# Kernel optimization log

Hardware: AMD Instinct MI355X
Metric: run time of the kernel (lower is better)

## Reference

```python
import jax, jax.numpy as jnp
import numpy as np

B, P, K = 8, 1024, 20          # clouds, points per cloud, knn neighbors
H, HD = 256, 512               # module hidden_dim, edge-MLP hidden (TransformerBlockRes default)
L, C = 3, 512                  # n_hidden_layers, n_components
N = B * P
LN_EPS = 1e-5


def _layer_norm(x, g, b):
    m = jnp.mean(x, axis=-1, keepdims=True)
    v = jnp.var(x, axis=-1, keepdims=True)
    return (x - m) * jax.lax.rsqrt(v + LN_EPS) * g + b


def _mlp(x, W1, b1, g1, be1, W2, b2, g2, be2):
    # Linear -> LayerNorm -> ELU -> Linear -> LayerNorm -> ELU (pos_nn / attn_nn)
    h = jax.nn.elu(_layer_norm(x @ W1 + b1, g1, be1))
    return jax.nn.elu(_layer_norm(h @ W2 + b2, g2, be2))


def _knn(pos):
    # knn_graph within each cloud, loop=False (self excluded). Equal-size clouds.
    p = pos.reshape(B, P, 3)
    d2 = jnp.sum((p[:, :, None, :] - p[:, None, :, :]) ** 2, axis=-1)  # [B,P,P]
    d2 = d2 + jnp.eye(P, dtype=d2.dtype) * 1e10                        # exclude self
    idx = jax.lax.top_k(-d2, K)[1]                                     # [B,P,K]
    return (idx + (jnp.arange(B) * P)[:, None, None]).reshape(N, K)    # global ids


def setup_inputs() -> dict:
    key = jax.random.key(0)
    cnt = [0]

    def nrm(shape, scale):
        cnt[0] += 1
        return (jax.random.normal(jax.random.fold_in(key, cnt[0]), shape, dtype=jnp.float32) * scale)

    d = {}
    d["pos"] = nrm((N, 3), 1.0)
    d["batch"] = jnp.repeat(jnp.arange(B, dtype=jnp.int32), P)
    # stem Linear(3, H)
    d["ffm_W"] = nrm((3, H), 3 ** -0.5); d["ffm_b"] = jnp.zeros((H,), jnp.float32)
    # PointTransformerConv linears (no bias), stacked over L layers
    s = H ** -0.5
    d["lin_W"] = nrm((L, H, H), s); d["src_W"] = nrm((L, H, H), s); d["dst_W"] = nrm((L, H, H), s)
    # pos_nn: Linear(3,HD)+LN+ELU+Linear(HD,H)+LN+ELU
    d["pos1_W"] = nrm((L, 3, HD), 3 ** -0.5); d["pos1_b"] = jnp.zeros((L, HD), jnp.float32)
    d["pos_ln1_g"] = jnp.ones((L, HD), jnp.float32); d["pos_ln1_b"] = jnp.zeros((L, HD), jnp.float32)
    d["pos2_W"] = nrm((L, HD, H), HD ** -0.5); d["pos2_b"] = jnp.zeros((L, H), jnp.float32)
    d["pos_ln2_g"] = jnp.ones((L, H), jnp.float32); d["pos_ln2_b"] = jnp.zeros((L, H), jnp.float32)
    # attn_nn: Linear(H,HD)+LN+ELU+Linear(HD,H)+LN+ELU
    d["att1_W"] = nrm((L, H, HD), s); d["att1_b"] = jnp.zeros((L, HD), jnp.float32)
    d["att_ln1_g"] = jnp.ones((L, HD), jnp.float32); d["att_ln1_b"] = jnp.zeros((L, HD), jnp.float32)
    d["att2_W"] = nrm((L, HD, H), HD ** -0.5); d["att2_b"] = jnp.zeros((L, H), jnp.float32)
    d["att_ln2_g"] = jnp.ones((L, H), jnp.float32); d["att_ln2_b"] = jnp.zeros((L, H), jnp.float32)
    # per-layer tail: LayerNorm + ELU + Linear + ResidualCoefficient
    d["blk_ln_g"] = jnp.ones((L, H), jnp.float32); d["blk_ln_b"] = jnp.zeros((L, H), jnp.float32)
    d["blk_W"] = nrm((L, H, H), s); d["blk_b"] = jnp.zeros((L, H), jnp.float32)
    d["res_alpha"] = nrm((L,), 0.1)  # torch init is zeros; small random for a nontrivial test
    d["r1_W"] = nrm((H, H), s); d["r1_b"] = jnp.zeros((H,), jnp.float32)
    d["r2_W"] = nrm((H, H), s); d["r2_b"] = jnp.zeros((H,), jnp.float32)
    d["r2_ln_g"] = jnp.ones((H,), jnp.float32); d["r2_ln_b"] = jnp.zeros((H,), jnp.float32)
    d["r3_W"] = nrm((H, H), s); d["r3_b"] = jnp.zeros((H,), jnp.float32)
    d["r3_ln_g"] = jnp.ones((H,), jnp.float32); d["r3_ln_b"] = jnp.zeros((H,), jnp.float32)
    d["r4_W"] = nrm((H, C), s); d["r4_b"] = jnp.zeros((C,), jnp.float32)
    return d


def reference(pos, batch, ffm_W, ffm_b, lin_W, src_W, dst_W,
              pos1_W, pos1_b, pos_ln1_g, pos_ln1_b, pos2_W, pos2_b, pos_ln2_g, pos_ln2_b,
              att1_W, att1_b, att_ln1_g, att_ln1_b, att2_W, att2_b, att_ln2_g, att_ln2_b,
              blk_ln_g, blk_ln_b, blk_W, blk_b, res_alpha,
              r1_W, r1_b, r2_W, r2_b, r2_ln_g, r2_ln_b, r3_W, r3_b, r3_ln_g, r3_ln_b, r4_W, r4_b):
    # knn graph is identical every layer (pos never changes) -> compute once
    neigh = _knn(pos)                       # [N,K] neighbor (source) ids j for each target i
    rel = pos[:, None, :] - pos[neigh]      # pos_i - pos_j, [N,K,3]
    x = pos @ ffm_W + ffm_b                 # [N,H]
    for i in range(L):
        a_src = x @ src_W[i]                # [N,H]
        a_dst = x @ dst_W[i]
        v = x @ lin_W[i]
        delta = _mlp(rel, pos1_W[i], pos1_b[i], pos_ln1_g[i], pos_ln1_b[i],
                     pos2_W[i], pos2_b[i], pos_ln2_g[i], pos_ln2_b[i])          # [N,K,H]
        alpha = _mlp(a_dst[:, None, :] - a_src[neigh] + delta,
                     att1_W[i], att1_b[i], att_ln1_g[i], att_ln1_b[i],
                     att2_W[i], att2_b[i], att_ln2_g[i], att_ln2_b[i])          # [N,K,H]
        attn = jax.nn.softmax(alpha, axis=1)                                    # per-channel over K neighbors
        agg = jnp.sum(attn * (v[neigh] + delta), axis=1)                        # sum aggregation (PyG default)
        h = jax.nn.elu(_layer_norm(agg, blk_ln_g[i], blk_ln_b[i])) @ blk_W[i] + blk_b[i]
        x = x + res_alpha[i] * h
    h = x @ r1_W + r1_b                                                         # [N,H]
    pooled = jax.ops.segment_max(h, batch, num_segments=B)                      # global_max_pool [B,H]
    h = jax.nn.elu(_layer_norm(pooled @ r2_W + r2_b, r2_ln_g, r2_ln_b))
    h = jax.nn.elu(_layer_norm(h @ r3_W + r3_b, r3_ln_g, r3_ln_b))
    return h @ r4_W + r4_b                                                      # [B,C]
```

## Files before the change

kernel.cpp:

```cpp
#include <hip/hip_runtime.h>
#include <math.h>

#define NPTS 8192
#define PPC  1024
#define BCL  8
#define KNN  20
#define HDIM 256
#define HD2  512
#define NL   3
#define NCOMP 512
#define EDG  (NPTS*KNN)
#define QS   768

typedef __bf16 bf16x8 __attribute__((ext_vector_type(8)));
typedef float f32x4 __attribute__((ext_vector_type(4)));
typedef unsigned int uint4v __attribute__((ext_vector_type(4)));
typedef unsigned short us8 __attribute__((ext_vector_type(8)));

__device__ inline unsigned short f2bf(float f) {
  unsigned u = __float_as_uint(f);
  u += 0x7FFF + ((u >> 16) & 1);
  return (unsigned short)(u >> 16);
}
__device__ inline unsigned short f2bf_fast(float f) {
  return (unsigned short)((__float_as_uint(f) + 0x8000u) >> 16);
}
__device__ inline unsigned pack2bf(float a, float b) {
#if __has_builtin(__builtin_amdgcn_cvt_pk_bf16_f32)
  auto t = __builtin_amdgcn_cvt_pk_bf16_f32(a, b);
  return __builtin_bit_cast(unsigned, t);
#else
  return ((__float_as_uint(a) + 0x8000u) >> 16) |
         ((__float_as_uint(b) + 0x8000u) & 0xFFFF0000u);
#endif
}
__device__ inline float bf2f(unsigned short u) {
  return __uint_as_float((unsigned)u << 16);
}
__device__ inline float elu(float y) { return (y > 0.f) ? y : (__expf(y) - 1.f); }

__global__ __launch_bounds__(256)
void knn_wave(const float* __restrict__ pos, int* __restrict__ neigh,
              float* __restrict__ rel_f) {
  __shared__ float px[PPC], py[PPC], pz[PPC];
  int tid = threadIdx.x;
  int i0 = blockIdx.x * 4;
  int base = i0 & ~(PPC - 1);
  for (int t = tid; t < PPC; t += 256) {
    px[t] = pos[(size_t)(base + t) * 3 + 0];
    py[t] = pos[(size_t)(base + t) * 3 + 1];
    pz[t] = pos[(size_t)(base + t) * 3 + 2];
  }
  __syncthreads();
  int wave = tid >> 6, lane = tid & 63;
  int i = i0 + wave;
  int il = i - base;
  float xi = px[il], yi = py[il], zi = pz[il];
  float d[16];
  #pragma unroll
  for (int q = 0; q < 16; ++q) {
    int t = lane + 64 * q;
    float dx = xi - px[t], dy = yi - py[t], dz = zi - pz[t];
    float dd = dx * dx + dy * dy + dz * dz;
    d[q] = (t == il) ? 3.4e38f : dd;
  }
  int mywin = 0;
  for (int k = 0; k < KNN; ++k) {
    float v = d[0]; int idx = lane;
    #pragma unroll
    for (int q = 1; q < 16; ++q)
      if (d[q] < v) { v = d[q]; idx = q * 64 + lane; }
    #pragma unroll
    for (int off = 1; off < 64; off <<= 1) {
      float ov = __shfl_xor(v, off, 64);
      int oi = __shfl_xor(idx, off, 64);
      if (ov < v || (ov == v && oi < idx)) { v = ov; idx = oi; }
    }
    if (lane == k) mywin = idx;
    int qwin = idx >> 6;
    bool own = (idx & 63) == lane;
    #pragma unroll
    for (int q = 0; q < 16; ++q)
      if (own && q == qwin) d[q] = 3.4e38f;
  }
  if (lane < KNN) {
    neigh[(size_t)i * KNN + lane] = base + mywin;
    size_t rb = ((size_t)i * KNN + lane) * 3;
    rel_f[rb + 0] = xi - px[mywin];
    rel_f[rb + 1] = yi - py[mywin];
    rel_f[rb + 2] = zi - pz[mywin];
  }
}

__global__ __launch_bounds__(256)
void transpose_w(const float* __restrict__ W, unsigned short* __restrict__ out,
                 int K, int N, int Kpad) {
  int n = blockIdx.x;
  for (int k = threadIdx.x; k < Kpad; k += 256)
    out[(size_t)n * Kpad + k] = (k < K) ? f2bf(W[(size_t)k * N + n]) : (unsigned short)0;
}

__global__ __launch_bounds__(64)
void pack_w(const float* __restrict__ W, unsigned short* __restrict__ out, int N) {
  int blk = blockIdx.x;
  int NT = N / 16;
  int ks = blk / NT, nt = blk % NT;
  int lane = threadIdx.x;
  int l16 = lane & 15, quad = lane >> 4;
  int col = nt * 16 + l16;
  int krow = ks * 32 + quad * 8;
  unsigned short o[8];
  #pragma unroll
  for (int j = 0; j < 8; ++j)
    o[j] = f2bf(W[(size_t)(krow + j) * N + col]);
  *(uint4v*)&out[((size_t)blk * 64 + lane) * 8] = *(uint4v*)o;
}

__global__ __launch_bounds__(256)
void prep_pos(const float* __restrict__ pos, unsigned short* __restrict__ posb) {
  int idx = blockIdx.x * 256 + threadIdx.x;
  int m = idx >> 5, c = idx & 31;
  posb[idx] = (c < 3) ? f2bf(pos[(size_t)m * 3 + c]) : (unsigned short)0;
}

__global__ __launch_bounds__(256)
void pos_fused(const float* __restrict__ rel_f, const float* __restrict__ W1,
               const float* __restrict__ b1, const float* __restrict__ g1,
               const float* __restrict__ be1,
               const unsigned short* __restrict__ B2p, const float* __restrict__ bias2,
               const float* __restrict__ g2, const float* __restrict__ be2,
               unsigned short* __restrict__ delta_b, int edge_base) {
  __shared__ alignas(16) char smem[46464];
  unsigned short* H = (unsigned short*)smem;
  float* w1s = (float*)(smem + 33280);
  float* b1s = w1s + 1536;
  float* g1s = b1s + 512;
  float* be1s = g1s + 512;
  float* lnsum = (float*)(smem + 45568);
  float* lnsq = lnsum + 64;
  float* relS = (float*)(smem + 46080);
  int tid = threadIdx.x;
  int wave = tid >> 6, lane = tid & 63;
  int el0 = blockIdx.x * 32;
  int eg0 = edge_base + el0;
  for (int t = tid; t < 1536; t += 256) w1s[t] = W1[t];
  for (int t = tid; t < 512; t += 256) { b1s[t] = b1[t]; g1s[t] = g1[t]; be1s[t] = be1[t]; }
  if (tid < 96) relS[tid] = rel_f[(size_t)eg0 * 3 + tid];
  __syncthreads();
  {
    int rIW = lane >> 3, sub = lane & 7;
    int row = wave * 8 + rIW;
    float r0 = relS[row * 3 + 0], r1v = relS[row * 3 + 1], r2v = relS[row * 3 + 2];
    int cb = sub * 64;
    float h[64]; float s = 0.f, sq = 0.f;
    #pragma unroll
    for (int cc = 0; cc < 16; ++cc) {
      f32x4 w0 = *(const f32x4*)&w1s[cb + cc * 4];
      f32x4 wa = *(const f32x4*)&w1s[512 + cb + cc * 4];
      f32x4 wb = *(const f32x4*)&w1s[1024 + cb + cc * 4];
      f32x4 bb = *(const f32x4*)&b1s[cb + cc * 4];
      #pragma unroll
      for (int q = 0; q < 4; ++q) {
        float hv = fmaf(r0, w0[q], fmaf(r1v, wa[q], fmaf(r2v, wb[q], bb[q])));
        h[cc * 4 + q] = hv; s += hv; sq += hv * hv;
      }
    }
    #pragma unroll
    for (int off = 1; off < 8; off <<= 1) { s += __shfl_xor(s, off, 64); sq += __shfl_xor(sq, off, 64); }
    float mean = s * (1.f / 512.f);
    float var = sq * (1.f / 512.f) - mean * mean;
    float rr = rsqrtf(var + 1e-5f);
    #pragma unroll
    for (int cc = 0; cc < 8; ++cc) {
      unsigned u[4];
      #pragma unroll
      for (int q = 0; q < 4; ++q) {
        int c0 = cb + cc * 8 + 2 * q;
        float y0 = elu((h[cc * 8 + 2 * q]     - mean) * rr * g1s[c0]     + be1s[c0]);
        float y1 = elu((h[cc * 8 + 2 * q + 1] - mean) * rr * g1s[c0 + 1] + be1s[c0 + 1]);
        u[q] = pack2bf(y0, y1);
      }
      *(uint4v*)&H[row * 520 + cb + cc * 8] = *(uint4v*)u;
    }
  }
  __syncthreads();
  int quad = lane >> 4, l16 = lane & 15;
  int wm2 = (wave >> 1) * 16, wn2 = (wave & 1) * 128, wni = wave & 1;
  int nb2 = (wave & 1) * 8;
  f32x4 acc2[8] = {};
  for (int k0 = 0; k0 < 512; k0 += 32) {
    int ks = k0 >> 5;
    bf16x8 bvv[8];
    #pragma unroll
    for (int ni = 0; ni < 8; ++ni)
      bvv[ni] = *(const bf16x8*)(B2p + ((size_t)(ks * 16 + nb2 + ni) * 64 + lane) * 8);
    bf16x8 a2 = __builtin_bit_cast(bf16x8, *(const uint4v*)&H[(wm2 + l16) * 520 + k0 + quad * 8]);
    #pragma unroll
    for (int ni = 0; ni < 8; ++ni)
      acc2[ni] = __builtin_amdgcn_mfma_f32_16x16x32_bf16(a2, bvv[ni], acc2[ni], 0, 0, 0);
  }
  #pragma unroll
  for (int r = 0; r < 4; ++r) {
    int row = wm2 + quad * 4 + r;
    float s2 = 0.f, q2 = 0.f;
    #pragma unroll
    for (int ni = 0; ni < 8; ++ni) {
      float val = acc2[ni][r] + bias2[wn2 + ni * 16 + l16];
      acc2[ni][r] = val; s2 += val; q2 += val * val;
    }
    #pragma unroll
    for (int off = 1; off < 16; off <<= 1) { s2 += __shfl_xor(s2, off, 64); q2 += __shfl_xor(q2, off, 64); }
    if (l16 == 0) { lnsum[wni * 32 + row] = s2; lnsq[wni * 32 + row] = q2; }
  }
  __syncthreads();
  #pragma unroll
  for (int r = 0; r < 4; ++r) {
    int row = wm2 + quad * 4 + r;
    float tot = lnsum[row] + lnsum[32 + row];
    float tsq = lnsq[row] + lnsq[32 + row];
    float mean = tot * (1.f / 256.f);
    float var = tsq * (1.f / 256.f) - mean * mean;
    float rr = rsqrtf(var + 1e-5f);
    size_t ob = (size_t)(el0 + row) * 256;
    #pragma unroll
    for (int ni = 0; ni < 8; ++ni) {
      int col = wn2 + ni * 16 + l16;
      delta_b[ob + col] = f2bf_fast(elu((acc2[ni][r] - mean) * rr * g2[col] + be2[col]));
    }
  }
}

__global__ __launch_bounds__(256)
void attn_fused(const unsigned short* __restrict__ qkv,
                const unsigned short* __restrict__ delta_b,
                const int* __restrict__ neigh,
                const unsigned short* __restrict__ B1p, const float* __restrict__ bias1,
                const float* __restrict__ g1, const float* __restrict__ be1,
                const unsigned short* __restrict__ B2p, const float* __restrict__ bias2,
                const float* __restrict__ g2, const float* __restrict__ be2,
                unsigned short* __restrict__ alpha_b, int edge_base) {
  __shared__ alignas(16) char smem[34304];
  unsigned short* H = (unsigned short*)smem;
  float* lnsum = (float*)(smem + 33280);
  float* lnsq  = lnsum + 64;
  int* iS = (int*)(smem + 33792);
  int* jS = iS + 32;
  int tid = threadIdx.x;
  int wave = tid >> 6, lane = tid & 63;
  int quad = lane >> 4, l16 = lane & 15;
  int el0 = blockIdx.x * 32;
  int eg0 = edge_base + el0;
  if (tid < 32) { iS[tid] = (eg0 + tid) / KNN; jS[tid] = neigh[eg0 + tid]; }
  __syncthreads();
  int wm1 = (wave >> 1) * 16, wn1 = (wave & 1) * 256, wni = wave & 1;
  int nb1 = (wave & 1) * 16;
  us8 areg[8];
  {
    int r = wm1 + l16;
    int i = iS[r], j = jS[r], e = el0 + r;
    const unsigned short* pdp = qkv + (size_t)i * QS + 256;
    const unsigned short* psp = qkv + (size_t)j * QS;
    const unsigned short* plp = delta_b + (size_t)e * 256;
    #pragma unroll
    for (int ks = 0; ks < 8; ++ks) {
      int c = ks * 32 + quad * 8;
      us8 pd = *(const us8*)(pdp + c);
      us8 ps = *(const us8*)(psp + c);
      us8 pl = *(const us8*)(plp + c);
      unsigned u[4];
      #pragma unroll
      for (int q = 0; q < 4; ++q)
        u[q] = pack2bf(bf2f(pd[2*q])   - bf2f(ps[2*q])   + bf2f(pl[2*q]),
                       bf2f(pd[2*q+1]) - bf2f(ps[2*q+1]) + bf2f(pl[2*q+1]));
      areg[ks] = __builtin_bit_cast(us8, *(uint4v*)u);
    }
  }
  f32x4 acc1[16] = {};
  #pragma unroll
  for (int ks = 0; ks < 8; ++ks) {
    bf16x8 bvv[16];
    #pragma unroll
    for (int ni = 0; ni < 16; ++ni)
      bvv[ni] = *(const bf16x8*)(B1p + ((size_t)(ks * 32 + nb1 + ni) * 64 + lane) * 8);
    bf16x8 a1 = __builtin_bit_cast(bf16x8, areg[ks]);
    #pragma unroll
    for (int ni = 0; ni < 16; ++ni)
      acc1[ni] = __builtin_amdgcn_mfma_f32_16x16x32_bf16(a1, bvv[ni], acc1[ni], 0, 0, 0);
  }
  #pragma unroll
  for (int r = 0; r < 4; ++r) {
    int row = wm1 + quad * 4 + r;
    float s = 0.f, sq = 0.f;
    #pragma unroll
    for (int ni = 0; ni < 16; ++ni) {
      float val = acc1[ni][r] + bias1[wn1 + ni * 16 + l16];
      acc1[ni][r] = val; s += val; sq += val * val;
    }
    #pragma unroll
    for (int off = 1; off < 16; off <<= 1) { s += __shfl_xor(s, off, 64); sq += __shfl_xor(sq, off, 64); }
    if (l16 == 0) { lnsum[wni * 32 + row] = s; lnsq[wni * 32 + row] = sq; }
  }
  __syncthreads();
  #pragma unroll
  for (int r = 0; r < 4; ++r) {
    int row = wm1 + quad * 4 + r;
    float tot = lnsum[row] + lnsum[32 + row];
    float tsq = lnsq[row] + lnsq[32 + row];
    float mean = tot * (1.f / 512.f);
    float var = tsq * (1.f / 512.f) - mean * mean;
    float rr = rsqrtf(var + 1e-5f);
    #pragma unroll
    for (int ni = 0; ni < 16; ++ni) {
      int col = wn1 + ni * 16 + l16;
      H[row * 520 + col] = f2bf_fast(elu((acc1[ni][r] - mean) * rr * g1[col] + be1[col]));
    }
  }
  __syncthreads();
  int wm2 = (wave >> 1) * 16, wn2 = (wave & 1) * 128;
  int nb2 = (wave & 1) * 8;
  f32x4 acc2[8] = {};
  for (int k0 = 0; k0 < 512; k0 += 32) {
    int ks = k0 >> 5;
    bf16x8 bvv[8];
    #pragma unroll
    for (int ni = 0; ni < 8; ++ni)
      bvv[ni] = *(const bf16x8*)(B2p + ((size_t)(ks * 16 + nb2 + ni) * 64 + lane) * 8);
    bf16x8 a2 = __builtin_bit_cast(bf16x8, *(const uint4v*)&H[(wm2 + l16) * 520 + k0 + quad * 8]);
    #pragma unroll
    for (int ni = 0; ni < 8; ++ni)
      acc2[ni] = __builtin_amdgcn_mfma_f32_16x16x32_bf16(a2, bvv[ni], acc2[ni], 0, 0, 0);
  }
  #pragma unroll
  for (int r = 0; r < 4; ++r) {
    int row = wm2 + quad * 4 + r;
    float s2 = 0.f, q2 = 0.f;
    #pragma unroll
    for (int ni = 0; ni < 8; ++ni) {
      float val = acc2[ni][r] + bias2[wn2 + ni * 16 + l16];
      acc2[ni][r] = val; s2 += val; q2 += val * val;
    }
    #pragma unroll
    for (int off = 1; off < 16; off <<= 1) { s2 += __shfl_xor(s2, off, 64); q2 += __shfl_xor(q2, off, 64); }
    if (l16 == 0) { lnsum[wni * 32 + row] = s2; lnsq[wni * 32 + row] = q2; }
  }
  __syncthreads();
  #pragma unroll
  for (int r = 0; r < 4; ++r) {
    int row = wm2 + quad * 4 + r;
    float tot = lnsum[row] + lnsum[32 + row];
    float tsq = lnsq[row] + lnsq[32 + row];
    float mean = tot * (1.f / 256.f);
    float var = tsq * (1.f / 256.f) - mean * mean;
    float rr = rsqrtf(var + 1e-5f);
    size_t ob = (size_t)(el0 + row) * 256;
    #pragma unroll
    for (int ni = 0; ni < 8; ++ni) {
      int col = wn2 + ni * 16 + l16;
      alpha_b[ob + col] = f2bf_fast(elu((acc2[ni][r] - mean) * rr * g2[col] + be2[col]));
    }
  }
}

#define APAD 40
__global__ __launch_bounds__(256)
void gemm_mfma(const unsigned short* __restrict__ A, const unsigned short* __restrict__ Bt,
               const float* __restrict__ bias, float* __restrict__ Cf,
               unsigned short* __restrict__ Cb, int M, int Nn, int Kk) {
  __shared__ alignas(16) unsigned short As[128 * APAD];
  __shared__ alignas(16) unsigned short Bs[128 * APAD];
  int tid = threadIdx.x;
  int wave = tid >> 6, lane = tid & 63;
  int quad = lane >> 4, l16 = lane & 15;
  int wm = (wave >> 1) * 64, wn = (wave & 1) * 64;
  int m0 = blockIdx.y * 128, n0 = blockIdx.x * 128;
  f32x4 acc[4][4] = {};
  int srow = tid >> 2;
  int scol = (tid & 3) * 8;
  for (int k0 = 0; k0 < Kk; k0 += 32) {
    #pragma unroll
    for (int h = 0; h < 2; ++h) {
      int r = srow + h * 64;
      int gm = m0 + r;
      uint4v va = {0, 0, 0, 0};
      if (gm < M) va = *(const uint4v*)(A + (size_t)gm * Kk + k0 + scol);
      *(uint4v*)(&As[r * APAD + scol]) = va;
      int gn = n0 + r;
      uint4v vb = *(const uint4v*)(Bt + (size_t)gn * Kk + k0 + scol);
      *(uint4v*)(&Bs[r * APAD + scol]) = vb;
    }
    __syncthreads();
    bf16x8 af[4], bfr[4];
    #pragma unroll
    for (int mi = 0; mi < 4; ++mi)
      af[mi] = __builtin_bit_cast(bf16x8, *(const uint4v*)(&As[(wm + mi * 16 + l16) * APAD + quad * 8]));
    #pragma unroll
    for (int ni = 0; ni < 4; ++ni)
      bfr[ni] = __builtin_bit_cast(bf16x8, *(const uint4v*)(&Bs[(wn + ni * 16 + l16) * APAD + quad * 8]));
    #pragma unroll
    for (int mi = 0; mi < 4; ++mi)
      #pragma unroll
      for (int ni = 0; ni < 4; ++ni)
        acc[mi][ni] = __builtin_amdgcn_mfma_f32_16x16x32_bf16(af[mi], bfr[ni], acc[mi][ni], 0, 0, 0);
    __syncthreads();
  }
  float bvs[4]; int gns[4];
  #pragma unroll
  for (int ni = 0; ni < 4; ++ni) {
    gns[ni] = n0 + wn + ni * 16 + l16;
    bvs[ni] = bias ? bias[gns[ni]] : 0.f;
  }
  #pragma unroll
  for (int mi = 0; mi < 4; ++mi) {
    #pragma unroll
    for (int r = 0; r < 4; ++r) {
      int gm = m0 + wm + mi * 16 + quad * 4 + r;
      if (gm >= M) continue;
      #pragma unroll
      for (int ni = 0; ni < 4; ++ni) {
        float val = acc[mi][ni][r] + bvs[ni];
        if (Cf) Cf[(size_t)gm * Nn + gns[ni]] = val;
        if (Cb) Cb[(size_t)gm * Nn + gns[ni]] = f2bf_fast(val);
      }
    }
  }
}

#define BM0 64
#define BN0 64
#define BK0 16
__global__ __launch_bounds__(256)
void gemm_bias(const float* __restrict__ A, const float* __restrict__ Bw,
               const float* __restrict__ bias, float* __restrict__ C,
               int M, int Nn, int Kk) {
  __shared__ float Asm[BK0][BM0 + 1];
  __shared__ float Bsm[BK0][BN0 + 1];
  int bm = blockIdx.y * BM0, bn = blockIdx.x * BN0;
  int tid = threadIdx.x;
  int tx = tid & 15, ty = tid >> 4;
  float acc[4][4] = {{0.f}};
  for (int k0 = 0; k0 < Kk; k0 += BK0) {
    #pragma unroll
    for (int ii = 0; ii < 4; ++ii) {
      int e = tid + ii * 256;
      int m = e >> 4, k = e & 15;
      int gm = bm + m, gk = k0 + k;
      Asm[k][m] = (gm < M && gk < Kk) ? A[(size_t)gm * Kk + gk] : 0.f;
    }
    #pragma unroll
    for (int ii = 0; ii < 4; ++ii) {
      int e = tid + ii * 256;
      int k = e >> 6, n = e & 63;
      int gk = k0 + k, gn = bn + n;
      Bsm[k][n] = (gk < Kk && gn < Nn) ? Bw[(size_t)gk * Nn + gn] : 0.f;
    }
    __syncthreads();
    #pragma unroll
    for (int kk = 0; kk < BK0; ++kk) {
      float a[4], b[4];
      #pragma unroll
      for (int ii = 0; ii < 4; ++ii) a[ii] = Asm[kk][ty * 4 + ii];
      #pragma unroll
      for (int jj = 0; jj < 4; ++jj) b[jj] = Bsm[kk][tx * 4 + jj];
      #pragma unroll
      for (int ii = 0; ii < 4; ++ii)
        #pragma unroll
        for (int jj = 0; jj < 4; ++jj)
          acc[ii][jj] += a[ii] * b[jj];
    }
    __syncthreads();
  }
  #pragma unroll
  for (int ii = 0; ii < 4; ++ii) {
    int gm = bm + ty * 4 + ii;
    if (gm >= M) continue;
    #pragma unroll
    for (int jj = 0; jj < 4; ++jj) {
      int gn = bn + tx * 4 + jj;
      if (gn >= Nn) continue;
      float vv = acc[ii][jj];
      if (bias) vv += bias[gn];
      C[(size_t)gm * Nn + gn] = vv;
    }
  }
}

__global__ __launch_bounds__(256)
void ln_elu_kernel(const float* __restrict__ in, float* __restrict__ outf,
                   unsigned short* __restrict__ outb,
                   const float* __restrict__ g, const float* __restrict__ bb,
                   int Cn, int do_elu) {
  __shared__ float sdata[4];
  size_t row = blockIdx.x;
  const float* x = in + row * Cn;
  int tid = threadIdx.x;
  float v0 = x[tid];
  float v1 = (Cn == 512) ? x[tid + 256] : 0.f;
  float s = v0 + v1;
  #pragma unroll
  for (int off = 32; off > 0; off >>= 1) s += __shfl_xor(s, off, 64);
  if ((tid & 63) == 0) sdata[tid >> 6] = s;
  __syncthreads();
  float mean = (sdata[0] + sdata[1] + sdata[2] + sdata[3]) / (float)Cn;
  float d0 = v0 - mean;
  float d1 = (Cn == 512) ? (v1 - mean) : 0.f;
  float sq = d0 * d0 + d1 * d1;
  __syncthreads();
  #pragma unroll
  for (int off = 32; off > 0; off >>= 1) sq += __shfl_xor(sq, off, 64);
  if ((tid & 63) == 0) sdata[tid >> 6] = sq;
  __syncthreads();
  float var = (sdata[0] + sdata[1] + sdata[2] + sdata[3]) / (float)Cn;
  float r = rsqrtf(var + 1e-5f);
  float y0 = d0 * r * g[tid] + bb[tid];
  if (do_elu) y0 = elu(y0);
  if (outf) outf[row * Cn + tid] = y0;
  if (outb) outb[row * Cn + tid] = f2bf_fast(y0);
  if (Cn == 512) {
    float y1 = d1 * r * g[tid + 256] + bb[tid + 256];
    if (do_elu) y1 = elu(y1);
    if (outf) outf[row * Cn + tid + 256] = y1;
    if (outb) outb[row * Cn + tid + 256] = f2bf_fast(y1);
  }
}

__global__ __launch_bounds__(256)
void softmax_agg(const unsigned short* __restrict__ alpha_b,
                 const unsigned short* __restrict__ delta_b,
                 const unsigned short* __restrict__ qkv,
                 const int* __restrict__ neigh,
                 float* __restrict__ agg, int node0) {
  int nl = blockIdx.x;
  int c = threadIdx.x;
  int i = node0 + nl;
  float av[KNN];
  float mx = -3.4e38f;
  #pragma unroll
  for (int k = 0; k < KNN; ++k) {
    av[k] = bf2f(alpha_b[((size_t)nl * KNN + k) * HDIM + c]);
    mx = fmaxf(mx, av[k]);
  }
  float ssum = 0.f;
  #pragma unroll
  for (int k = 0; k < KNN; ++k) { av[k] = __expf(av[k] - mx); ssum += av[k]; }
  float inv = 1.f / ssum;
  float acc = 0.f;
  #pragma unroll
  for (int k = 0; k < KNN; ++k) {
    int j = neigh[(size_t)i * KNN + k];
    acc += av[k] * inv * (bf2f(qkv[(size_t)j * QS + 512 + c]) +
                          bf2f(delta_b[((size_t)nl * KNN + k) * HDIM + c]));
  }
  agg[(size_t)i * HDIM + c] = acc;
}

__global__ __launch_bounds__(256)
void axpy_res(float* __restrict__ x, unsigned short* __restrict__ xb,
              const float* __restrict__ h, const float* __restrict__ alpha, int l) {
  size_t idx = (size_t)blockIdx.x * 256 + threadIdx.x;
  float nv = x[idx] + alpha[l] * h[idx];
  x[idx] = nv;
  xb[idx] = f2bf_fast(nv);
}

__global__ __launch_bounds__(256)
void seg_max_p(const float* __restrict__ h, float* __restrict__ part) {
  int blk = blockIdx.x;
  int b = blk >> 4, ch = blk & 15;
  int c = threadIdx.x;
  const float* base = h + ((size_t)b * PPC + (size_t)ch * 64) * HDIM;
  float m = -3.4e38f;
  for (int p = 0; p < 64; ++p)
    m = fmaxf(m, base[(size_t)p * HDIM + c]);
  part[(size_t)blk * HDIM + c] = m;
}
__global__ __launch_bounds__(256)
void seg_max_f(const float* __restrict__ part, float* __restrict__ pooled) {
  int b = blockIdx.x;
  int c = threadIdx.x;
  float m = -3.4e38f;
  for (int k = 0; k < 16; ++k)
    m = fmaxf(m, part[(size_t)(b * 16 + k) * HDIM + c]);
  pooled[(size_t)b * HDIM + c] = m;
}

extern "C" void kernel_launch(void* const* d_in, const int* in_sizes, int n_in,
                              void* d_out, int out_size, void* d_ws, size_t ws_size,
                              hipStream_t stream) {
  const float* pos       = (const float*)d_in[0];
  const float* ffm_W     = (const float*)d_in[2];
  const float* ffm_b     = (const float*)d_in[3];
  const float* lin_W     = (const float*)d_in[4];
  const float* src_W     = (const float*)d_in[5];
  const float* dst_W     = (const float*)d_in[6];
  const float* pos1_W    = (const float*)d_in[7];
  const float* pos1_b    = (const float*)d_in[8];
  const float* pos_ln1_g = (const float*)d_in[9];
  const float* pos_ln1_b = (const float*)d_in[10];
  const float* pos2_W    = (const float*)d_in[11];
  const float* pos2_b    = (const float*)d_in[12];
  const float* pos_ln2_g = (const float*)d_in[13];
  const float* pos_ln2_b = (const float*)d_in[14];
  const float* att1_W    = (const float*)d_in[15];
  const float* att1_b    = (const float*)d_in[16];
  const float* att_ln1_g = (const float*)d_in[17];
  const float* att_ln1_b = (const float*)d_in[18];
  const float* att2_W    = (const float*)d_in[19];
  const float* att2_b    = (const float*)d_in[20];
  const float* att_ln2_g = (const float*)d_in[21];
  const float* att_ln2_b = (const float*)d_in[22];
  const float* blk_ln_g  = (const float*)d_in[23];
  const float* blk_ln_b  = (const float*)d_in[24];
  const float* blk_W     = (const float*)d_in[25];
  const float* blk_b     = (const float*)d_in[26];
  const float* res_alpha = (const float*)d_in[27];
  const float* r1_W = (const float*)d_in[28]; const float* r1_b = (const float*)d_in[29];
  const float* r2_W = (const float*)d_in[30]; const float* r2_b = (const float*)d_in[31];
  const float* r2_ln_g = (const float*)d_in[32]; const float* r2_ln_b = (const float*)d_in[33];
  const float* r3_W = (const float*)d_in[34]; const float* r3_b = (const float*)d_in[35];
  const float* r3_ln_g = (const float*)d_in[36]; const float* r3_ln_b = (const float*)d_in[37];
  const float* r4_W = (const float*)d_in[38]; const float* r4_b = (const float*)d_in[39];
  float* out = (float*)d_out;

  char* wsp = (char*)d_ws;
  auto alloc = [&](size_t bytes) -> void* {
    void* p = (void*)wsp;
    wsp += (bytes + 255) & ~(size_t)255;
    return p;
  };
  int*            neigh   = (int*)alloc(EDG * sizeof(int));
  float*          rel_f   = (float*)alloc((size_t)EDG * 3 * 4);
  unsigned short* posb    = (unsigned short*)alloc((size_t)NPTS * 32 * 2);
  float*          x       = (float*)alloc((size_t)NPTS * HDIM * 4);
  unsigned short* xb      = (unsigned short*)alloc((size_t)NPTS * HDIM * 2);
  unsigned short* xln_b   = (unsigned short*)alloc((size_t)NPTS * HDIM * 2);
  unsigned short* qkv     = (unsigned short*)alloc((size_t)NPTS * QS * 2);
  float*          agg     = (float*)alloc((size_t)NPTS * HDIM * 4);
  float*          segp    = (float*)alloc((size_t)128 * HDIM * 4);
  float*          pooled  = (float*)alloc((size_t)BCL * HDIM * 4);
  float*          hh      = (float*)alloc((size_t)BCL * HDIM * 4);
  unsigned short* ffmt = (unsigned short*)alloc((size_t)HDIM * 32 * 2);
  unsigned short* r1t  = (unsigned short*)alloc((size_t)HDIM * HDIM * 2);
  unsigned short *qkvt[NL], *blkt[NL];
  unsigned short *pos2p[NL], *att1p[NL], *att2p[NL];
  for (int l = 0; l < NL; ++l) {
    qkvt[l]  = (unsigned short*)alloc((size_t)QS * HDIM * 2);
    blkt[l]  = (unsigned short*)alloc((size_t)HDIM * HDIM * 2);
    pos2p[l] = (unsigned short*)alloc((size_t)HDIM * HD2 * 2);
    att1p[l] = (unsigned short*)alloc((size_t)HD2 * HDIM * 2);
    att2p[l] = (unsigned short*)alloc((size_t)HDIM * HD2 * 2);
  }
  size_t used = (size_t)(wsp - (char*)d_ws);
  size_t avail = (ws_size > used) ? (ws_size - used) : 0;
  size_t per_node = (size_t)KNN * (HDIM * 2 * 2) + 1024;
  int Nc = (int)(avail / per_node);
  if (Nc > NPTS) Nc = NPTS;
  Nc &= ~15;
  if (Nc < 16) Nc = 16;
  unsigned short* delta_b = (unsigned short*)alloc((size_t)Nc * KNN * HDIM * 2);
  unsigned short* alpha_b = (unsigned short*)alloc((size_t)Nc * KNN * HDIM * 2);

  auto mgemm = [&](const unsigned short* A, const unsigned short* Bt, const float* bias,
                   float* Cf, unsigned short* Cb, int M, int Nn, int Kk) {
    dim3 g(Nn / 128, (M + 127) / 128);
    gemm_mfma<<<g, dim3(256), 0, stream>>>(A, Bt, bias, Cf, Cb, M, Nn, Kk);
  };
  auto fgemm = [&](const float* A, const float* Bw, const float* bias, float* Cp,
                   int M, int Nn, int Kk) {
    dim3 g((Nn + BN0 - 1) / BN0, (M + BM0 - 1) / BM0);
    gemm_bias<<<g, dim3(256), 0, stream>>>(A, Bw, bias, Cp, M, Nn, Kk);
  };

  transpose_w<<<HDIM, 256, 0, stream>>>(ffm_W, ffmt, 3, HDIM, 32);
  transpose_w<<<HDIM, 256, 0, stream>>>(r1_W, r1t, HDIM, HDIM, HDIM);
  for (int l = 0; l < NL; ++l) {
    transpose_w<<<HDIM, 256, 0, stream>>>(src_W + (size_t)l * HDIM * HDIM, qkvt[l], HDIM, HDIM, HDIM);
    transpose_w<<<HDIM, 256, 0, stream>>>(dst_W + (size_t)l * HDIM * HDIM, qkvt[l] + 256 * 256, HDIM, HDIM, HDIM);
    transpose_w<<<HDIM, 256, 0, stream>>>(lin_W + (size_t)l * HDIM * HDIM, qkvt[l] + 512 * 256, HDIM, HDIM, HDIM);
    transpose_w<<<HDIM, 256, 0, stream>>>(blk_W + (size_t)l * HDIM * HDIM, blkt[l], HDIM, HDIM, HDIM);
    pack_w<<<(HD2 / 32) * (HDIM / 16), 64, 0, stream>>>(pos2_W + (size_t)l * HD2 * HDIM, pos2p[l], HDIM);
    pack_w<<<(HDIM / 32) * (HD2 / 16), 64, 0, stream>>>(att1_W + (size_t)l * HDIM * HD2, att1p[l], HD2);
    pack_w<<<(HD2 / 32) * (HDIM / 16), 64, 0, stream>>>(att2_W + (size_t)l * HD2 * HDIM, att2p[l], HDIM);
  }

  knn_wave<<<NPTS / 4, 256, 0, stream>>>(pos, neigh, rel_f);
  prep_pos<<<NPTS * 32 / 256, 256, 0, stream>>>(pos, posb);
  mgemm(posb, ffmt, ffm_b, x, xb, NPTS, HDIM, 32);

  for (int l = 0; l < NL; ++l) {
    mgemm(xb, qkvt[l], nullptr, nullptr, qkv, NPTS, QS, HDIM);

    for (int n0 = 0; n0 < NPTS; n0 += Nc) {
      int nc = (Nc < NPTS - n0) ? Nc : (NPTS - n0);
      int ec = nc * KNN;
      pos_fused<<<ec / 32, 256, 0, stream>>>(
          rel_f, pos1_W + (size_t)l * 3 * HD2, pos1_b + (size_t)l * HD2,
          pos_ln1_g + (size_t)l * HD2, pos_ln1_b + (size_t)l * HD2,
          pos2p[l], pos2_b + (size_t)l * HDIM,
          pos_ln2_g + (size_t)l * HDIM, pos_ln2_b + (size_t)l * HDIM,
          delta_b, n0 * KNN);
      attn_fused<<<ec / 32, 256, 0, stream>>>(
          qkv, delta_b, neigh,
          att1p[l], att1_b + (size_t)l * HD2,
          att_ln1_g + (size_t)l * HD2, att_ln1_b + (size_t)l * HD2,
          att2p[l], att2_b + (size_t)l * HDIM,
          att_ln2_g + (size_t)l * HDIM, att_ln2_b + (size_t)l * HDIM,
          alpha_b, n0 * KNN);
      softmax_agg<<<nc, 256, 0, stream>>>(alpha_b, delta_b, qkv, neigh, agg, n0);
    }
    ln_elu_kernel<<<NPTS, 256, 0, stream>>>(agg, nullptr, xln_b,
                                            blk_ln_g + (size_t)l * HDIM, blk_ln_b + (size_t)l * HDIM, HDIM, 1);
    mgemm(xln_b, blkt[l], blk_b + (size_t)l * HDIM, agg, nullptr, NPTS, HDIM, HDIM);
    axpy_res<<<(NPTS * HDIM) / 256, 256, 0, stream>>>(x, xb, agg, res_alpha, l);
  }

  mgemm(xb, r1t, r1_b, agg, nullptr, NPTS, HDIM, HDIM);
  seg_max_p<<<128, 256, 0, stream>>>(agg, segp);
  seg_max_f<<<BCL, 256, 0, stream>>>(segp, pooled);
  fgemm(pooled, r2_W, r2_b, hh, BCL, HDIM, HDIM);
  ln_elu_kernel<<<BCL, 256, 0, stream>>>(hh, hh, nullptr, r2_ln_g, r2_ln_b, HDIM, 1);
  fgemm(hh, r3_W, r3_b, pooled, BCL, HDIM, HDIM);
  ln_elu_kernel<<<BCL, 256, 0, stream>>>(pooled, pooled, nullptr, r3_ln_g, r3_ln_b, HDIM, 1);
  fgemm(pooled, r4_W, r4_b, out, BCL, NCOMP, HDIM);
}
```

Before: 1.948 ms.

## Retile edge-MLP GEMMs so each wave covers all rows, halving weight loads

The wave-to-tile mapping in pos_fused and attn_fused changes. Each wave now owns a column strip across all 32 rows, so each B-fragment load from global memory feeds two MFMAs instead of one, which cuts weight traffic per block. attn_fused now stages the gathered A operand in shared memory, adding an extra barrier and more LDS use that may reduce occupancy. The LayerNorm partial sums now reduce across four waves, per-column bias and gamma values are held in registers, and pack2bf drops the hardware cvt builtin for the integer rounding path.

```diff
diff --git a/kernel.cpp b/kernel.cpp
--- a/kernel.cpp
+++ b/kernel.cpp
@@ -26,13 +26,8 @@
   return (unsigned short)((__float_as_uint(f) + 0x8000u) >> 16);
 }
 __device__ inline unsigned pack2bf(float a, float b) {
-#if __has_builtin(__builtin_amdgcn_cvt_pk_bf16_f32)
-  auto t = __builtin_amdgcn_cvt_pk_bf16_f32(a, b);
-  return __builtin_bit_cast(unsigned, t);
-#else
   return ((__float_as_uint(a) + 0x8000u) >> 16) |
          ((__float_as_uint(b) + 0x8000u) & 0xFFFF0000u);
-#endif
 }
 __device__ inline float bf2f(unsigned short u) {
   return __uint_as_float((unsigned)u << 16);
@@ -130,15 +125,15 @@
                const unsigned short* __restrict__ B2p, const float* __restrict__ bias2,
                const float* __restrict__ g2, const float* __restrict__ be2,
                unsigned short* __restrict__ delta_b, int edge_base) {
-  __shared__ alignas(16) char smem[46464];
+  __shared__ alignas(16) char smem[46976];
   unsigned short* H = (unsigned short*)smem;
   float* w1s = (float*)(smem + 33280);
   float* b1s = w1s + 1536;
   float* g1s = b1s + 512;
   float* be1s = g1s + 512;
   float* lnsum = (float*)(smem + 45568);
-  float* lnsq = lnsum + 64;
-  float* relS = (float*)(smem + 46080);
+  float* lnsq  = (float*)(smem + 46080);
+  float* relS  = (float*)(smem + 46592);
   int tid = threadIdx.x;
   int wave = tid >> 6, lane = tid & 63;
   int el0 = blockIdx.x * 32;
@@ -185,49 +180,60 @@
   }
   __syncthreads();
   int quad = lane >> 4, l16 = lane & 15;
-  int wm2 = (wave >> 1) * 16, wn2 = (wave & 1) * 128, wni = wave & 1;
-  int nb2 = (wave & 1) * 8;
-  f32x4 acc2[8] = {};
-  for (int k0 = 0; k0 < 512; k0 += 32) {
-    int ks = k0 >> 5;
-    bf16x8 bvv[8];
-    #pragma unroll
-    for (int ni = 0; ni < 8; ++ni)
-      bvv[ni] = *(const bf16x8*)(B2p + ((size_t)(ks * 16 + nb2 + ni) * 64 + lane) * 8);
-    bf16x8 a2 = __builtin_bit_cast(bf16x8, *(const uint4v*)&H[(wm2 + l16) * 520 + k0 + quad * 8]);
-    #pragma unroll
-    for (int ni = 0; ni < 8; ++ni)
-      acc2[ni] = __builtin_amdgcn_mfma_f32_16x16x32_bf16(a2, bvv[ni], acc2[ni], 0, 0, 0);
-  }
-  #pragma unroll
-  for (int r = 0; r < 4; ++r) {
-    int row = wm2 + quad * 4 + r;
-    float s2 = 0.f, q2 = 0.f;
-    #pragma unroll
-    for (int ni = 0; ni < 8; ++ni) {
-      float val = acc2[ni][r] + bias2[wn2 + ni * 16 + l16];
-      acc2[ni][r] = val; s2 += val; q2 += val * val;
-    }
-    #pragma unroll
-    for (int off = 1; off < 16; off <<= 1) { s2 += __shfl_xor(s2, off, 64); q2 += __shfl_xor(q2, off, 64); }
-    if (l16 == 0) { lnsum[wni * 32 + row] = s2; lnsq[wni * 32 + row] = q2; }
-  }
-  __syncthreads();
-  #pragma unroll
-  for (int r = 0; r < 4; ++r) {
-    int row = wm2 + quad * 4 + r;
-    float tot = lnsum[row] + lnsum[32 + row];
-    float tsq = lnsq[row] + lnsq[32 + row];
-    float mean = tot * (1.f / 256.f);
-    float var = tsq * (1.f / 256.f) - mean * mean;
-    float rr = rsqrtf(var + 1e-5f);
-    size_t ob = (size_t)(el0 + row) * 256;
-    #pragma unroll
-    for (int ni = 0; ni < 8; ++ni) {
-      int col = wn2 + ni * 16 + l16;
-      delta_b[ob + col] = f2bf_fast(elu((acc2[ni][r] - mean) * rr * g2[col] + be2[col]));
-    }
-  }
+  int cb2 = wave * 64;
+  f32x4 acc2[2][4] = {};
+  #pragma unroll 4
+  for (int ks = 0; ks < 16; ++ks) {
+    bf16x8 bvv[4];
+    #pragma unroll
+    for (int ni = 0; ni < 4; ++ni)
+      bvv[ni] = *(const bf16x8*)(B2p + ((size_t)(ks * 16 + wave * 4 + ni) * 64 + lane) * 8);
+    bf16x8 a0 = __builtin_bit_cast(bf16x8, *(const uint4v*)&H[(l16) * 520 + ks * 32 + quad * 8]);
+    bf16x8 a1 = __builtin_bit_cast(bf16x8, *(const uint4v*)&H[(16 + l16) * 520 + ks * 32 + quad * 8]);
+    #pragma unroll
+    for (int ni = 0; ni < 4; ++ni) {
+      acc2[0][ni] = __builtin_amdgcn_mfma_f32_16x16x32_bf16(a0, bvv[ni], acc2[0][ni], 0, 0, 0);
+      acc2[1][ni] = __builtin_amdgcn_mfma_f32_16x16x32_bf16(a1, bvv[ni], acc2[1][ni], 0, 0, 0);
+    }
+  }
+  float b2v[4], g2v[4], be2v[4];
+  #pragma unroll
+  for (int ni = 0; ni < 4; ++ni) {
+    int col = cb2 + ni * 16 + l16;
+    b2v[ni] = bias2[col]; g2v[ni] = g2[col]; be2v[ni] = be2[col];
+  }
+  #pragma unroll
+  for (int mt = 0; mt < 2; ++mt)
+    #pragma unroll
+    for (int r = 0; r < 4; ++r) {
+      int row = mt * 16 + quad * 4 + r;
+      float s2 = 0.f, q2 = 0.f;
+      #pragma unroll
+      for (int ni = 0; ni < 4; ++ni) {
+        float val = acc2[mt][ni][r] + b2v[ni];
+        acc2[mt][ni][r] = val; s2 += val; q2 += val * val;
+      }
+      #pragma unroll
+      for (int off = 1; off < 16; off <<= 1) { s2 += __shfl_xor(s2, off, 64); q2 += __shfl_xor(q2, off, 64); }
+      if (l16 == 0) { lnsum[wave * 32 + row] = s2; lnsq[wave * 32 + row] = q2; }
+    }
+  __syncthreads();
+  #pragma unroll
+  for (int mt = 0; mt < 2; ++mt)
+    #pragma unroll
+    for (int r = 0; r < 4; ++r) {
+      int row = mt * 16 + quad * 4 + r;
+      float tot = lnsum[row] + lnsum[32 + row] + lnsum[64 + row] + lnsum[96 + row];
+      float tsq = lnsq[row] + lnsq[32 + row] + lnsq[64 + row] + lnsq[96 + row];
+      float mean = tot * (1.f / 256.f);
+      float var = tsq * (1.f / 256.f) - mean * mean;
+      float rr = rsqrtf(var + 1e-5f);
+      size_t ob = (size_t)(el0 + row) * 256;
+      #pragma unroll
+      for (int ni = 0; ni < 4; ++ni)
+        delta_b[ob + cb2 + ni * 16 + l16] =
+            f2bf_fast(elu((acc2[mt][ni][r] - mean) * rr * g2v[ni] + be2v[ni]));
+    }
 }
 
 __global__ __launch_bounds__(256)
@@ -239,12 +245,13 @@
                 const unsigned short* __restrict__ B2p, const float* __restrict__ bias2,
                 const float* __restrict__ g2, const float* __restrict__ be2,
                 unsigned short* __restrict__ alpha_b, int edge_base) {
-  __shared__ alignas(16) char smem[34304];
-  unsigned short* H = (unsigned short*)smem;
-  float* lnsum = (float*)(smem + 33280);
-  float* lnsq  = lnsum + 64;
-  int* iS = (int*)(smem + 33792);
-  int* jS = iS + 32;
+  __shared__ alignas(16) char smem[51456];
+  unsigned short* As = (unsigned short*)smem;
+  unsigned short* H  = (unsigned short*)(smem + 16896);
+  float* lnsum = (float*)(smem + 50176);
+  float* lnsq  = (float*)(smem + 50688);
+  int* iS = (int*)(smem + 51200);
+  int* jS = (int*)(smem + 51328);
   int tid = threadIdx.x;
   int wave = tid >> 6, lane = tid & 63;
   int quad = lane >> 4, l16 = lane & 15;
@@ -252,113 +259,136 @@
   int eg0 = edge_base + el0;
   if (tid < 32) { iS[tid] = (eg0 + tid) / KNN; jS[tid] = neigh[eg0 + tid]; }
   __syncthreads();
-  int wm1 = (wave >> 1) * 16, wn1 = (wave & 1) * 256, wni = wave & 1;
-  int nb1 = (wave & 1) * 16;
-  us8 areg[8];
   {
-    int r = wm1 + l16;
+    int r = tid & 31, seg = tid >> 5;
     int i = iS[r], j = jS[r], e = el0 + r;
-    const unsigned short* pdp = qkv + (size_t)i * QS + 256;
-    const unsigned short* psp = qkv + (size_t)j * QS;
-    const unsigned short* plp = delta_b + (size_t)e * 256;
-    #pragma unroll
-    for (int ks = 0; ks < 8; ++ks) {
-      int c = ks * 32 + quad * 8;
-      us8 pd = *(const us8*)(pdp + c);
-      us8 ps = *(const us8*)(psp + c);
-      us8 pl = *(const us8*)(plp + c);
+    int c0 = seg * 32;
+    #pragma unroll
+    for (int q4 = 0; q4 < 4; ++q4) {
+      int c = c0 + q4 * 8;
+      us8 pd = *(const us8*)(qkv + (size_t)i * QS + 256 + c);
+      us8 ps = *(const us8*)(qkv + (size_t)j * QS + c);
+      us8 pl = *(const us8*)(delta_b + (size_t)e * 256 + c);
       unsigned u[4];
       #pragma unroll
       for (int q = 0; q < 4; ++q)
         u[q] = pack2bf(bf2f(pd[2*q])   - bf2f(ps[2*q])   + bf2f(pl[2*q]),
                        bf2f(pd[2*q+1]) - bf2f(ps[2*q+1]) + bf2f(pl[2*q+1]));
-      areg[ks] = __builtin_bit_cast(us8, *(uint4v*)u);
-    }
-  }
-  f32x4 acc1[16] = {};
-  #pragma unroll
+      *(uint4v*)&As[r * 264 + c] = *(uint4v*)u;
+    }
+  }
+  __syncthreads();
+  int cb1 = wave * 128;
+  f32x4 acc1[2][8] = {};
+  #pragma unroll 2
   for (int ks = 0; ks < 8; ++ks) {
-    bf16x8 bvv[16];
-    #pragma unroll
-    for (int ni = 0; ni < 16; ++ni)
-      bvv[ni] = *(const bf16x8*)(B1p + ((size_t)(ks * 32 + nb1 + ni) * 64 + lane) * 8);
-    bf16x8 a1 = __builtin_bit_cast(bf16x8, areg[ks]);
-    #pragma unroll
-    for (int ni = 0; ni < 16; ++ni)
-      acc1[ni] = __builtin_amdgcn_mfma_f32_16x16x32_bf16(a1, bvv[ni], acc1[ni], 0, 0, 0);
-  }
-  #pragma unroll
-  for (int r = 0; r < 4; ++r) {
-    int row = wm1 + quad * 4 + r;
-    float s = 0.f, sq = 0.f;
-    #pragma unroll
-    for (int ni = 0; ni < 16; ++ni) {
-      float val = acc1[ni][r] + bias1[wn1 + ni * 16 + l16];
-      acc1[ni][r] = val; s += val; sq += val * val;
-    }
-    #pragma unroll
-    for (int off = 1; off < 16; off <<= 1) { s += __shfl_xor(s, off, 64); sq += __shfl_xor(sq, off, 64); }
-    if (l16 == 0) { lnsum[wni * 32 + row] = s; lnsq[wni * 32 + row] = sq; }
-  }
-  __syncthreads();
-  #pragma unroll
-  for (int r = 0; r < 4; ++r) {
-    int row = wm1 + quad * 4 + r;
-    float tot = lnsum[row] + lnsum[32 + row];
-    float tsq = lnsq[row] + lnsq[32 + row];
-    float mean = tot * (1.f / 512.f);
-    float var = tsq * (1.f / 512.f) - mean * mean;
-    float rr = rsqrtf(var + 1e-5f);
-    #pragma unroll
-    for (int ni = 0; ni < 16; ++ni) {
-      int col = wn1 + ni * 16 + l16;
-      H[row * 520 + col] = f2bf_fast(elu((acc1[ni][r] - mean) * rr * g1[col] + be1[col]));
-    }
-  }
-  __syncthreads();
-  int wm2 = (wave >> 1) * 16, wn2 = (wave & 1) * 128;
-  int nb2 = (wave & 1) * 8;
-  f32x4 acc2[8] = {};
-  for (int k0 = 0; k0 < 512; k0 += 32) {
-    int ks = k0 >> 5;
     bf16x8 bvv[8];
     #pragma unroll
     for (int ni = 0; ni < 8; ++ni)
-      bvv[ni] = *(const bf16x8*)(B2p + ((size_t)(ks * 16 + nb2 + ni) * 64 + lane) * 8);
-    bf16x8 a2 = __builtin_bit_cast(bf16x8, *(const uint4v*)&H[(wm2 + l16) * 520 + k0 + quad * 8]);
-    #pragma unroll
-    for (int ni = 0; ni < 8; ++ni)
-      acc2[ni] = __builtin_amdgcn_mfma_f32_16x16x32_bf16(a2, bvv[ni], acc2[ni], 0, 0, 0);
-  }
-  #pragma unroll
-  for (int r = 0; r < 4; ++r) {
-    int row = wm2 + quad * 4 + r;
-    float s2 = 0.f, q2 = 0.f;
+      bvv[ni] = *(const bf16x8*)(B1p + ((size_t)(ks * 32 + wave * 8 + ni) * 64 + lane) * 8);
+    bf16x8 a0 = __builtin_bit_cast(bf16x8, *(const uint4v*)&As[(l16) * 264 + ks * 32 + quad * 8]);
+    bf16x8 a1 = __builtin_bit_cast(bf16x8, *(const uint4v*)&As[(16 + l16) * 264 + ks * 32 + quad * 8]);
     #pragma unroll
     for (int ni = 0; ni < 8; ++ni) {
-      float val = acc2[ni][r] + bias2[wn2 + ni * 16 + l16];
-      acc2[ni][r] = val; s2 += val; q2 += val * val;
-    }
-    #pragma unroll
-    for (int off = 1; off < 16; off <<= 1) { s2 += __shfl_xor(s2, off, 64); q2 += __shfl_xor(q2, off, 64); }
-    if (l16 == 0) { lnsum[wni * 32 + row] = s2; lnsq[wni * 32 + row] = q2; }
-  }
-  __syncthreads();
-  #pragma unroll
-  for (int r = 0; r < 4; ++r) {
-    int row = wm2 + quad * 4 + r;
-    float tot = lnsum[row] + lnsum[32 + row];
-    float tsq = lnsq[row] + lnsq[32 + row];
-    float mean = tot * (1.f / 256.f);
-    float var = tsq * (1.f / 256.f) - mean * mean;
-    float rr = rsqrtf(var + 1e-5f);
-    size_t ob = (size_t)(el0 + row) * 256;
+      acc1[0][ni] = __builtin_amdgcn_mfma_f32_16x16x32_bf16(a0, bvv[ni], acc1[0][ni], 0, 0, 0);
+      acc1[1][ni] = __builtin_amdgcn_mfma_f32_16x16x32_bf16(a1, bvv[ni], acc1[1][ni], 0, 0, 0);
+    }
+  }
+  {
+    float b1v[8], g1v[8], be1v[8];
     #pragma unroll
     for (int ni = 0; ni < 8; ++ni) {
-      int col = wn2 + ni * 16 + l16;
-      alpha_b[ob + col] = f2bf_fast(elu((acc2[ni][r] - mean) * rr * g2[col] + be2[col]));
-    }
-  }
+      int col = cb1 + ni * 16 + l16;
+      b1v[ni] = bias1[col]; g1v[ni] = g1[col]; be1v[ni] = be1[col];
+    }
+    #pragma unroll
+    for (int mt = 0; mt < 2; ++mt)
+      #pragma unroll
+      for (int r = 0; r < 4; ++r) {
+        int row = mt * 16 + quad * 4 + r;
+        float s = 0.f, sq = 0.f;
+        #pragma unroll
+        for (int ni = 0; ni < 8; ++ni) {
+          float val = acc1[mt][ni][r] + b1v[ni];
+          acc1[mt][ni][r] = val; s += val; sq += val * val;
+        }
+        #pragma unroll
+        for (int off = 1; off < 16; off <<= 1) { s += __shfl_xor(s, off, 64); sq += __shfl_xor(sq, off, 64); }
+        if (l16 == 0) { lnsum[wave * 32 + row] = s; lnsq[wave * 32 + row] = sq; }
+      }
+    __syncthreads();
+    #pragma unroll
+    for (int mt = 0; mt < 2; ++mt)
+      #pragma unroll
+      for (int r = 0; r < 4; ++r) {
+        int row = mt * 16 + quad * 4 + r;
+        float tot = lnsum[row] + lnsum[32 + row] + lnsum[64 + row] + lnsum[96 + row];
+        float tsq = lnsq[row] + lnsq[32 + row] + lnsq[64 + row] + lnsq[96 + row];
+        float mean = tot * (1.f / 512.f);
+        float var = tsq * (1.f / 512.f) - mean * mean;
+        float rr = rsqrtf(var + 1e-5f);
+        #pragma unroll
+        for (int ni = 0; ni < 8; ++ni) {
+          int col = cb1 + ni * 16 + l16;
+          H[row * 520 + col] = f2bf_fast(elu((acc1[mt][ni][r] - mean) * rr * g1v[ni] + be1v[ni]));
+        }
+      }
+  }
+  __syncthreads();
+  int cb2 = wave * 64;
+  f32x4 acc2[2][4] = {};
+  #pragma unroll 4
+  for (int ks = 0; ks < 16; ++ks) {
+    bf16x8 bvv[4];
+    #pragma unroll
+    for (int ni = 0; ni < 4; ++ni)
+      bvv[ni] = *(const bf16x8*)(B2p + ((size_t)(ks * 16 + wave * 4 + ni) * 64 + lane) * 8);
+    bf16x8 a0 = __builtin_bit_cast(bf16x8, *(const uint4v*)&H[(l16) * 520 + ks * 32 + quad * 8]);
+    bf16x8 a1 = __builtin_bit_cast(bf16x8, *(const uint4v*)&H[(16 + l16) * 520 + ks * 32 + quad * 8]);
+    #pragma unroll
+    for (int ni = 0; ni < 4; ++ni) {
+      acc2[0][ni] = __builtin_amdgcn_mfma_f32_16x16x32_bf16(a0, bvv[ni], acc2[0][ni], 0, 0, 0);
+      acc2[1][ni] = __builtin_amdgcn_mfma_f32_16x16x32_bf16(a1, bvv[ni], acc2[1][ni], 0, 0, 0);
+    }
+  }
+  float b2v[4], g2v[4], be2v[4];
+  #pragma unroll
+  for (int ni = 0; ni < 4; ++ni) {
+    int col = cb2 + ni * 16 + l16;
+    b2v[ni] = bias2[col]; g2v[ni] = g2[col]; be2v[ni] = be2[col];
+  }
+  #pragma unroll
+  for (int mt = 0; mt < 2; ++mt)
+    #pragma unroll
+    for (int r = 0; r < 4; ++r) {
+      int row = mt * 16 + quad * 4 + r;
+      float s2 = 0.f, q2 = 0.f;
+      #pragma unroll
+      for (int ni = 0; ni < 4; ++ni) {
+        float val = acc2[mt][ni][r] + b2v[ni];
+        acc2[mt][ni][r] = val; s2 += val; q2 += val * val;
+      }
+      #pragma unroll
+      for (int off = 1; off < 16; off <<= 1) { s2 += __shfl_xor(s2, off, 64); q2 += __shfl_xor(q2, off, 64); }
+      if (l16 == 0) { lnsum[wave * 32 + row] = s2; lnsq[wave * 32 + row] = q2; }
+    }
+  __syncthreads();
+  #pragma unroll
+  for (int mt = 0; mt < 2; ++mt)
+    #pragma unroll
+    for (int r = 0; r < 4; ++r) {
+      int row = mt * 16 + quad * 4 + r;
+      float tot = lnsum[row] + lnsum[32 + row] + lnsum[64 + row] + lnsum[96 + row];
+      float tsq = lnsq[row] + lnsq[32 + row] + lnsq[64 + row] + lnsq[96 + row];
+      float mean = tot * (1.f / 256.f);
+      float var = tsq * (1.f / 256.f) - mean * mean;
+      float rr = rsqrtf(var + 1e-5f);
+      size_t ob = (size_t)(el0 + row) * 256;
+      #pragma unroll
+      for (int ni = 0; ni < 4; ++ni)
+        alpha_b[ob + cb2 + ni * 16 + l16] =
+            f2bf_fast(elu((acc2[mt][ni][r] - mean) * rr * g2v[ni] + be2v[ni]));
+    }
 }
 
 #define APAD 40
```

After: 1.877 ms. 3.6% less time.
